# Optimization experiments

Measured on AMD Instinct MI355X. Metric: run time of the kernel, lower is better.

Reference implementation:

```python
import jax, jax.numpy as jnp
import numpy as np

H = 32; D = 128; HID = 4096       # heads, head_dim, hidden
DOFF = 1024; BD = 32; T = DOFF + BD  # prefill tokens, decode batch, total tokens
MAXKV = 513; R = 16; NA = 4       # kv-cache slots, lora rank, num adapters
SCALE = 1.0 / float(np.sqrt(D))


def _add_lora(y, x, wa, wb, segment):
    # segmented (multi-tenant) LoRA: y[t] += x[t] @ A[aid(t)] @ B[aid(t)]
    t = x.shape[0]
    aid = jnp.clip(jnp.searchsorted(segment, jnp.arange(t), side='right') - 1, 0, NA - 1)
    oh = jax.nn.one_hot(aid, NA, dtype=x.dtype)           # [t, NA]
    u = jnp.einsum('th,ahr->atr', x, wa)                  # [NA, t, R]
    v = jnp.einsum('atr,arh->ath', u, wb)                 # [NA, t, HID]
    return y + jnp.einsum('ta,ath->th', oh, v)


def setup_inputs() -> dict:
    key = jax.random.key(0)
    ks = jax.random.split(key, 16)
    f = lambda k, s: (jax.random.normal(k, s, dtype=jnp.float32) * 0.02)
    inp = {
        'hidden_states': f(ks[0], (T, HID)),
        'Wq': f(ks[1], (HID, HID)), 'Wk': f(ks[2], (HID, HID)),
        'Wv': f(ks[3], (HID, HID)), 'Wo': f(ks[4], (HID, HID)),
        'wa_q': f(ks[5], (NA, HID, R)), 'wb_q': f(ks[6], (NA, R, HID)),
        'wa_k': f(ks[7], (NA, HID, R)), 'wb_k': f(ks[8], (NA, R, HID)),
        'wa_v': f(ks[9], (NA, HID, R)), 'wb_v': f(ks[10], (NA, R, HID)),
        'wa_o': f(ks[11], (NA, HID, R)), 'wb_o': f(ks[12], (NA, R, HID)),
        'k_cache': f(ks[13], (BD, MAXKV, H, D)),
        'v_cache': f(ks[14], (BD, MAXKV, H, D)),
        'indptr': jnp.array([0, 200, 456, 800, 1024], dtype=jnp.int32),
        'segment': jnp.array([0, 300, 600, 900, 1056], dtype=jnp.int32),
        'kv_lens': jax.random.randint(ks[15], (BD,), 0, 512, dtype=jnp.int32),
    }
    return inp


def reference(hidden_states, Wq, Wk, Wv, Wo, wa_q, wb_q, wa_k, wb_k, wa_v, wb_v,
              wa_o, wb_o, k_cache, v_cache, indptr, segment, kv_lens):
    # qkv proj + segmented LoRA add
    qp = _add_lora(hidden_states @ Wq, hidden_states, wa_q, wb_q, segment)
    kp = _add_lora(hidden_states @ Wk, hidden_states, wa_k, wb_k, segment)
    vp = _add_lora(hidden_states @ Wv, hidden_states, wa_v, wb_v, segment)

    # ---- ragged prefill attention (causal within each sequence) ----
    q = qp[:DOFF].reshape(DOFF, H, D)
    k = kp[:DOFF].reshape(DOFF, H, D)
    v = vp[:DOFF].reshape(DOFF, H, D)
    idx = jnp.arange(DOFF)
    seg = jnp.searchsorted(indptr, idx, side='right') - 1   # sequence id per token
    m = (seg[:, None] == seg[None, :]) & (idx[None, :] <= idx[:, None])
    s = jnp.einsum('qhd,khd->hqk', q, k) * SCALE
    p = jax.nn.softmax(jnp.where(m[None], s, -1e9), axis=-1)
    out_p = jnp.einsum('hqk,khd->qhd', p, v).reshape(DOFF, HID)

    # ---- paged decode attention (append new kv, attend over cache) ----
    qd = qp[DOFF:].reshape(BD, H, D)
    kd = kp[DOFF:].reshape(BD, H, D)
    vd = vp[DOFF:].reshape(BD, H, D)
    b = jnp.arange(BD)
    kc = k_cache.at[b, kv_lens].set(kd)
    vc = v_cache.at[b, kv_lens].set(vd)
    lens = kv_lens + 1
    md = jnp.arange(MAXKV)[None, :] < lens[:, None]          # [BD, MAXKV]
    sd = jnp.einsum('bhd,bkhd->bhk', qd, kc) * SCALE
    pd = jax.nn.softmax(jnp.where(md[:, None, :], sd, -1e9), axis=-1)
    out_d = jnp.einsum('bhk,bkhd->bhd', pd, vc).reshape(BD, HID)

    attn = jnp.concatenate([out_p, out_d], axis=0)           # [T, HID]
    o = _add_lora(attn @ Wo, attn, wa_o, wb_o, segment)
    return o
```

## Files before the change

kernel.cpp:

```cpp
#include <hip/hip_runtime.h>
#include <hip/hip_bf16.h>

#define H_     32
#define D_     128
#define HID_   4096
#define DOFF_  1024
#define BD_    32
#define T_     1056
#define MAXKV_ 513
#define R_     16
#define NA_    4
#define SCALE_ 0.08838834764831845f

typedef __attribute__((ext_vector_type(8))) short short8;
typedef __attribute__((ext_vector_type(4))) float f32x4;

__device__ __forceinline__ float toF(float x) { return x; }
__device__ __forceinline__ float toF(__hip_bfloat16 x) { return __bfloat162float(x); }
__device__ __forceinline__ void storev(float* p, float v) { *p = v; }
__device__ __forceinline__ void storev(__hip_bfloat16* p, float v) { *p = __float2bfloat16(v); }

__device__ __forceinline__ void gload16(const void* g, void* l) {
  __builtin_amdgcn_global_load_lds(
      (const __attribute__((address_space(1))) unsigned int*)g,
      (__attribute__((address_space(3))) unsigned int*)l, 16, 0, 0);
}

__device__ __forceinline__ void load4(const float* p, float* v) {
  float4 t = *(const float4*)p;
  v[0] = t.x; v[1] = t.y; v[2] = t.z; v[3] = t.w;
}
__device__ __forceinline__ void load4(const __hip_bfloat16* p, float* v) {
  short4 t = *(const short4*)p;
  const __hip_bfloat16* e = (const __hip_bfloat16*)&t;
  v[0] = toF(e[0]); v[1] = toF(e[1]); v[2] = toF(e[2]); v[3] = toF(e[3]);
}

__global__ __launch_bounds__(256) void cast_bf16_kernel(
    const float* __restrict__ X, __hip_bfloat16* __restrict__ Y, int n4) {
  int i = blockIdx.x * 256 + threadIdx.x;
  if (i >= n4) return;
  float4 v = ((const float4*)X)[i];
  __hip_bfloat16 o[4] = {__float2bfloat16(v.x), __float2bfloat16(v.y),
                         __float2bfloat16(v.z), __float2bfloat16(v.w)};
  *(short4*)(Y + (size_t)i * 4) = *(short4*)o;
}

__global__ __launch_bounds__(256) void transpose_cast4_kernel(
    const float* __restrict__ W0, const float* __restrict__ W1,
    const float* __restrict__ W2, const float* __restrict__ W3,
    __hip_bfloat16* __restrict__ WT4) {
  __shared__ float tile[64][65];
  const float* W = blockIdx.z == 0 ? W0 : (blockIdx.z == 1 ? W1
                   : (blockIdx.z == 2 ? W2 : W3));
  __hip_bfloat16* WT = WT4 + (size_t)blockIdx.z * HID_ * HID_;
  int tx = threadIdx.x & 15;
  int ty = threadIdx.x >> 4;
  int r0 = blockIdx.y * 64, c0 = blockIdx.x * 64;
#pragma unroll
  for (int s = 0; s < 64; s += 16) {
    float4 v = *(const float4*)(W + (size_t)(r0 + ty + s) * HID_ + c0 + tx * 4);
    tile[ty + s][tx * 4 + 0] = v.x;
    tile[ty + s][tx * 4 + 1] = v.y;
    tile[ty + s][tx * 4 + 2] = v.z;
    tile[ty + s][tx * 4 + 3] = v.w;
  }
  __syncthreads();
#pragma unroll
  for (int s = 0; s < 64; s += 16) {
    int c = ty + s;
    __hip_bfloat16 o[4];
#pragma unroll
    for (int e = 0; e < 4; ++e) o[e] = __float2bfloat16(tile[tx * 4 + e][c]);
    *(short4*)(WT + (size_t)(c0 + c) * HID_ + r0 + tx * 4) = *(short4*)o;
  }
}

template <typename XT>
__global__ __launch_bounds__(256) void lora_u_kernel(
    const XT* __restrict__ X, const float* __restrict__ WA0,
    const float* __restrict__ WA1, const float* __restrict__ WA2,
    const int* __restrict__ segment, float* __restrict__ U0,
    float* __restrict__ U1, float* __restrict__ U2) {
  int t = blockIdx.x;
  int tid = threadIdx.x;
  const float* WA = blockIdx.y == 0 ? WA0 : (blockIdx.y == 1 ? WA1 : WA2);
  float* U = blockIdx.y == 0 ? U0 : (blockIdx.y == 1 ? U1 : U2);

  int aid = 0;
#pragma unroll
  for (int i = 1; i < NA_; ++i)
    if (t >= segment[i]) aid = i;

  const XT* x = X + (size_t)t * HID_;
  const float* wa = WA + (size_t)aid * HID_ * R_;

  float part[R_];
#pragma unroll
  for (int r = 0; r < R_; ++r) part[r] = 0.f;

  for (int h = tid * 4; h < HID_; h += 1024) {
    float xv[4];
    load4(x + h, xv);
#pragma unroll
    for (int e = 0; e < 4; ++e) {
      const float* w = wa + (size_t)(h + e) * R_;
#pragma unroll
      for (int r = 0; r < R_; ++r) part[r] += xv[e] * w[r];
    }
  }

  __shared__ float red[256][R_ + 1];
#pragma unroll
  for (int r = 0; r < R_; ++r) red[tid][r] = part[r];
  __syncthreads();
  for (int s = 128; s > 0; s >>= 1) {
    if (tid < s) {
#pragma unroll
      for (int r = 0; r < R_; ++r) red[tid][r] += red[tid + s][r];
    }
    __syncthreads();
  }
  if (tid < R_) U[(size_t)t * R_ + tid] = red[0][tid];
}

template <typename OUT_T>
__global__ __launch_bounds__(256) void gemm_bf16_lora_kernel(
    const __hip_bfloat16* __restrict__ Xb, const __hip_bfloat16* __restrict__ WT4,
    const float* __restrict__ U0, const float* __restrict__ U1,
    const float* __restrict__ U2, const float* __restrict__ B0,
    const float* __restrict__ B1, const float* __restrict__ B2,
    const int* __restrict__ segment, OUT_T* __restrict__ Y0,
    OUT_T* __restrict__ Y1, OUT_T* __restrict__ Y2, int Trows) {
  __shared__ __hip_bfloat16 As[128 * 32];
  __shared__ __hip_bfloat16 Bs[128 * 32];

  const int nwg = gridDim.x * gridDim.y;
  const int flat = blockIdx.y * gridDim.x + blockIdx.x;
  const int swz = (flat & 7) * (nwg >> 3) + (flat >> 3);
  const int bx = swz % gridDim.x;
  const int by = swz / gridDim.x;
  const int w = bx >> 5;
  const int n0 = (bx & 31) * 128;
  const int m0 = by * 128;

  const __hip_bfloat16* WT = WT4 + (size_t)w * HID_ * HID_;
  const float* U = w == 0 ? U0 : (w == 1 ? U1 : U2);
  const float* BMAT = w == 0 ? B0 : (w == 1 ? B1 : B2);
  OUT_T* Y = w == 0 ? Y0 : (w == 1 ? Y1 : Y2);

  const int tid = threadIdx.x;
  const int lane = tid & 63;
  const int wave = tid >> 6;
  const int wr = (wave >> 1) * 64;
  const int wc = (wave & 1) * 64;

  const int srow = tid >> 2;
  const int sel = (tid & 3) * 8;
  int ar0 = m0 + srow;      if (ar0 >= Trows) ar0 = Trows - 1;
  int ar1 = m0 + srow + 64; if (ar1 >= Trows) ar1 = Trows - 1;
  const __hip_bfloat16* gA0 = Xb + (size_t)ar0 * HID_ + sel;
  const __hip_bfloat16* gA1 = Xb + (size_t)ar1 * HID_ + sel;
  const __hip_bfloat16* gB0 = WT + (size_t)(n0 + srow) * HID_ + sel;
  const __hip_bfloat16* gB1 = WT + (size_t)(n0 + srow + 64) * HID_ + sel;
  __hip_bfloat16* lA = As + tid * 8;
  __hip_bfloat16* lB = Bs + tid * 8;

  const int lrow = lane & 15;
  const int lk = (lane >> 4) * 8;
  const __hip_bfloat16* fA = As + (wr + lrow) * 32 + lk;
  const __hip_bfloat16* fB = Bs + (wc + lrow) * 32 + lk;

  f32x4 acc[4][4] = {};

  for (int k0 = 0; k0 < HID_; k0 += 32) {
    gload16(gA0, lA);
    gload16(gA1, lA + 2048);
    gload16(gB0, lB);
    gload16(gB1, lB + 2048);
    gA0 += 32; gA1 += 32; gB0 += 32; gB1 += 32;
    __syncthreads();
    short8 a[4], b[4];
#pragma unroll
    for (int mi = 0; mi < 4; ++mi) a[mi] = *(const short8*)(fA + mi * 512);
#pragma unroll
    for (int ni = 0; ni < 4; ++ni) b[ni] = *(const short8*)(fB + ni * 512);
#pragma unroll
    for (int mi = 0; mi < 4; ++mi)
#pragma unroll
      for (int ni = 0; ni < 4; ++ni)
        acc[mi][ni] = __builtin_amdgcn_mfma_f32_16x16x32_bf16(a[mi], b[ni], acc[mi][ni], 0, 0, 0);
    __syncthreads();
  }

  const int crow = (lane >> 4) * 4;
  const int ccol = lane & 15;
#pragma unroll
  for (int mi = 0; mi < 4; ++mi) {
    const int tb = m0 + wr + mi * 16 + crow;
#pragma unroll
    for (int i = 0; i < 4; ++i) {
      const int t = tb + i;
      if (t >= Trows) continue;
      int aid = 0;
#pragma unroll
      for (int s = 1; s < NA_; ++s)
        if (t >= segment[s]) aid = s;
      const float* ub = U + (size_t)t * R_;
      const float* bb = BMAT + (size_t)aid * R_ * HID_;
#pragma unroll
      for (int ni = 0; ni < 4; ++ni) {
        const int n = n0 + wc + ni * 16 + ccol;
        float v = acc[mi][ni][i];
        const float* bc = bb + n;
#pragma unroll
        for (int r = 0; r < R_; ++r) v += ub[r] * bc[(size_t)r * HID_];
        storev(Y + (size_t)t * HID_ + n, v);
      }
    }
  }
}

#define QB 64
#define KB 32

__global__ __launch_bounds__(256) void attn_prefill_mfma_kernel(
    const __hip_bfloat16* __restrict__ qp, const __hip_bfloat16* __restrict__ kp,
    const __hip_bfloat16* __restrict__ vp, const int* __restrict__ indptr,
    __hip_bfloat16* __restrict__ attn) {
  __shared__ __hip_bfloat16 Klds[KB * 128];
  __shared__ __hip_bfloat16 Vt[128 * 40];
  __shared__ __hip_bfloat16 Plds[4][16 * 40];

  const int nwg = gridDim.x * gridDim.y;
  const int flat = blockIdx.y * gridDim.x + blockIdx.x;
  const int swz = (flat & 7) * (nwg >> 3) + (flat >> 3);
  const int q0 = (swz % gridDim.x) * QB;
  const int h = swz / gridDim.x;

  const int tid = threadIdx.x;
  const int lane = tid & 63;
  const int wave = tid >> 6;
  const int g = lane >> 4;
  const int lc = lane & 15;

  int qrows[4], qstart[4];
#pragma unroll
  for (int i = 0; i < 4; ++i) {
    int q = q0 + wave * 16 + g * 4 + i;
    qrows[i] = q;
    int s0 = 0;
#pragma unroll
    for (int j = 1; j < NA_; ++j)
      if (q >= indptr[j]) s0 = indptr[j];
    qstart[i] = s0;
  }

  short8 aq[4];
  {
    const __hip_bfloat16* qrow = qp + (size_t)(q0 + wave * 16 + lc) * HID_ + h * D_;
#pragma unroll
    for (int dc = 0; dc < 4; ++dc)
      aq[dc] = *(const short8*)(qrow + dc * 32 + g * 8);
  }

  float mrow[4], lrow[4];
#pragma unroll
  for (int i = 0; i < 4; ++i) { mrow[i] = -1e30f; lrow[i] = 0.f; }
  f32x4 o[8] = {};

  int ks0 = 0;
#pragma unroll
  for (int j = 1; j < NA_; ++j)
    if (q0 >= indptr[j]) ks0 = indptr[j];
  const int kt0 = ks0 & ~(KB - 1);

  const int sr = tid >> 4;
  const int sc = tid & 15;

  for (int kt = kt0; kt < q0 + QB; kt += KB) {
    gload16(kp + (size_t)(kt + sr) * HID_ + h * D_ + ((sc ^ (sr & 7)) * 8),
            Klds + tid * 8);
    gload16(kp + (size_t)(kt + 16 + sr) * HID_ + h * D_ + ((sc ^ (sr & 7)) * 8),
            Klds + 2048 + tid * 8);
    {
      short8 v0 = *(const short8*)(vp + (size_t)(kt + sr) * HID_ + h * D_ + sc * 8);
      short8 v1 = *(const short8*)(vp + (size_t)(kt + 16 + sr) * HID_ + h * D_ + sc * 8);
      const __hip_bfloat16* e0 = (const __hip_bfloat16*)&v0;
      const __hip_bfloat16* e1 = (const __hip_bfloat16*)&v1;
#pragma unroll
      for (int e = 0; e < 8; ++e) {
        Vt[(sc * 8 + e) * 40 + sr] = e0[e];
        Vt[(sc * 8 + e) * 40 + sr + 16] = e1[e];
      }
    }
    __syncthreads();

    f32x4 s0v = {}, s1v = {};
#pragma unroll
    for (int dc = 0; dc < 4; ++dc) {
      const int cb = dc * 4 + g;
      short8 bk0 = *(const short8*)(Klds + lc * 128 + ((cb ^ (lc & 7)) * 8));
      short8 bk1 = *(const short8*)(Klds + (16 + lc) * 128 + ((cb ^ (lc & 7)) * 8));
      s0v = __builtin_amdgcn_mfma_f32_16x16x32_bf16(aq[dc], bk0, s0v, 0, 0, 0);
      s1v = __builtin_amdgcn_mfma_f32_16x16x32_bf16(aq[dc], bk1, s1v, 0, 0, 0);
    }

    const int kl0 = kt + lc, kl1 = kt + 16 + lc;
#pragma unroll
    for (int i = 0; i < 4; ++i) {
      float sm0 = s0v[i] * SCALE_;
      float sm1 = s1v[i] * SCALE_;
      bool v0ok = (kl0 >= qstart[i]) && (kl0 <= qrows[i]);
      bool v1ok = (kl1 >= qstart[i]) && (kl1 <= qrows[i]);
      float mx = fmaxf(v0ok ? sm0 : -1e30f, v1ok ? sm1 : -1e30f);
#pragma unroll
      for (int off = 1; off < 16; off <<= 1)
        mx = fmaxf(mx, __shfl_xor(mx, off));
      float mnew = fmaxf(mrow[i], mx);
      float alpha = __expf(mrow[i] - mnew);
      float p0 = v0ok ? __expf(sm0 - mnew) : 0.f;
      float p1 = v1ok ? __expf(sm1 - mnew) : 0.f;
      lrow[i] = lrow[i] * alpha + p0 + p1;
      mrow[i] = mnew;
#pragma unroll
      for (int dc = 0; dc < 8; ++dc) o[dc][i] *= alpha;
      Plds[wave][(g * 4 + i) * 40 + lc] = __float2bfloat16(p0);
      Plds[wave][(g * 4 + i) * 40 + 16 + lc] = __float2bfloat16(p1);
    }

    asm volatile("s_waitcnt lgkmcnt(0)" ::: "memory");

    short8 ap = *(const short8*)(&Plds[wave][lc * 40 + g * 8]);
#pragma unroll
    for (int dc = 0; dc < 8; ++dc) {
      short8 bv = *(const short8*)(&Vt[(dc * 16 + lc) * 40 + g * 8]);
      o[dc] = __builtin_amdgcn_mfma_f32_16x16x32_bf16(ap, bv, o[dc], 0, 0, 0);
    }
    __syncthreads();
  }

#pragma unroll
  for (int i = 0; i < 4; ++i) {
    float l = lrow[i];
#pragma unroll
    for (int off = 1; off < 16; off <<= 1) l += __shfl_xor(l, off);
    lrow[i] = 1.f / l;
  }
#pragma unroll
  for (int dc = 0; dc < 8; ++dc)
#pragma unroll
    for (int i = 0; i < 4; ++i)
      attn[(size_t)qrows[i] * HID_ + h * D_ + dc * 16 + lc] =
          __float2bfloat16(o[dc][i] * lrow[i]);
}

__global__ __launch_bounds__(256) void attn_decode_kernel(
    const __hip_bfloat16* __restrict__ qp, const __hip_bfloat16* __restrict__ kp,
    const __hip_bfloat16* __restrict__ vp, const float* __restrict__ kcache,
    const float* __restrict__ vcache, const int* __restrict__ kv_lens,
    __hip_bfloat16* __restrict__ attn) {
  int h = blockIdx.x;
  int b = blockIdx.y;
  int wave = threadIdx.x >> 6;
  int lane = threadIdx.x & 63;
  int t = DOFF_ + b;

  const __hip_bfloat16* qptr = qp + (size_t)t * HID_ + h * D_;
  float q0 = toF(qptr[lane]), q1 = toF(qptr[lane + 64]);
  int len = kv_lens[b];

  int cnt = len + 1;
  int chunk = (cnt + 3) >> 2;
  int ks = wave * chunk;
  int ke = ks + chunk; if (ke > cnt) ke = cnt;

  float m = -1e30f, l = 0.f, acc0 = 0.f, acc1 = 0.f;
  for (int k = ks; k < ke; ++k) {
    float kv0, kv1, vv0, vv1;
    if (k == len) {
      const __hip_bfloat16* kptr = kp + (size_t)t * HID_ + h * D_;
      const __hip_bfloat16* vptr = vp + (size_t)t * HID_ + h * D_;
      kv0 = toF(kptr[lane]); kv1 = toF(kptr[lane + 64]);
      vv0 = toF(vptr[lane]); vv1 = toF(vptr[lane + 64]);
    } else {
      size_t base = (((size_t)b * MAXKV_ + k) * H_ + h) * D_;
      kv0 = kcache[base + lane]; kv1 = kcache[base + lane + 64];
      vv0 = vcache[base + lane]; vv1 = vcache[base + lane + 64];
    }
    float s = q0 * kv0 + q1 * kv1;
#pragma unroll
    for (int off = 32; off > 0; off >>= 1) s += __shfl_xor(s, off);
    s *= SCALE_;
    float mnew = fmaxf(m, s);
    float alpha = __expf(m - mnew);
    float p = __expf(s - mnew);
    acc0 = acc0 * alpha + p * vv0;
    acc1 = acc1 * alpha + p * vv1;
    l = l * alpha + p;
    m = mnew;
  }

  __shared__ float sm[4], sl[4], sacc[4][128];
  if (lane == 0) { sm[wave] = m; sl[wave] = l; }
  sacc[wave][lane] = acc0;
  sacc[wave][lane + 64] = acc1;
  __syncthreads();
  if (wave == 0) {
    float M = fmaxf(fmaxf(sm[0], sm[1]), fmaxf(sm[2], sm[3]));
    float L = 0.f, A0 = 0.f, A1 = 0.f;
#pragma unroll
    for (int w = 0; w < 4; ++w) {
      float sc = __expf(sm[w] - M);
      L += sl[w] * sc;
      A0 += sacc[w][lane] * sc;
      A1 += sacc[w][lane + 64] * sc;
    }
    float inv = 1.f / L;
    __hip_bfloat16* outp = attn + (size_t)t * HID_ + h * D_;
    storev(outp + lane, A0 * inv);
    storev(outp + lane + 64, A1 * inv);
  }
}

extern "C" void kernel_launch(void* const* d_in, const int* in_sizes, int n_in,
                              void* d_out, int out_size, void* d_ws, size_t ws_size,
                              hipStream_t stream) {
  const float* hidden  = (const float*)d_in[0];
  const float* Wq      = (const float*)d_in[1];
  const float* Wk      = (const float*)d_in[2];
  const float* Wv      = (const float*)d_in[3];
  const float* Wo      = (const float*)d_in[4];
  const float* wa_q    = (const float*)d_in[5];
  const float* wb_q    = (const float*)d_in[6];
  const float* wa_k    = (const float*)d_in[7];
  const float* wb_k    = (const float*)d_in[8];
  const float* wa_v    = (const float*)d_in[9];
  const float* wb_v    = (const float*)d_in[10];
  const float* wa_o    = (const float*)d_in[11];
  const float* wb_o    = (const float*)d_in[12];
  const float* k_cache = (const float*)d_in[13];
  const float* v_cache = (const float*)d_in[14];
  const int*   indptr  = (const int*)d_in[15];
  const int*   segment = (const int*)d_in[16];
  const int*   kv_lens = (const int*)d_in[17];
  float* out = (float*)d_out;

  const size_t PROJ = (size_t)T_ * HID_;
  __hip_bfloat16* Xb    = (__hip_bfloat16*)d_ws;
  __hip_bfloat16* qp    = Xb + PROJ;
  __hip_bfloat16* kp    = qp + PROJ;
  __hip_bfloat16* vp    = kp + PROJ;
  __hip_bfloat16* attnb = vp + PROJ;
  __hip_bfloat16* WT4   = attnb + PROJ;
  float* u_q = (float*)(WT4 + 4 * (size_t)HID_ * HID_);
  float* u_k = u_q + (size_t)T_ * R_;
  float* u_v = u_k + (size_t)T_ * R_;
  float* u_o = u_v + (size_t)T_ * R_;

  const int n4 = (int)(PROJ / 4);

  cast_bf16_kernel<<<(n4 + 255) / 256, 256, 0, stream>>>(hidden, Xb, n4);
  transpose_cast4_kernel<<<dim3(HID_ / 64, HID_ / 64, 4), 256, 0, stream>>>(
      Wq, Wk, Wv, Wo, WT4);
  lora_u_kernel<float><<<dim3(T_, 3), 256, 0, stream>>>(
      hidden, wa_q, wa_k, wa_v, segment, u_q, u_k, u_v);

  gemm_bf16_lora_kernel<__hip_bfloat16><<<dim3(96, 9), 256, 0, stream>>>(
      Xb, WT4, u_q, u_k, u_v, wb_q, wb_k, wb_v, segment, qp, kp, vp, T_);

  attn_prefill_mfma_kernel<<<dim3(DOFF_ / QB, H_), 256, 0, stream>>>(qp, kp, vp, indptr, attnb);
  attn_decode_kernel<<<dim3(H_, BD_), 256, 0, stream>>>(qp, kp, vp, k_cache, v_cache,
                                                        kv_lens, attnb);

  lora_u_kernel<__hip_bfloat16><<<dim3(T_, 1), 256, 0, stream>>>(
      attnb, wa_o, wa_o, wa_o, segment, u_o, u_o, u_o);
  gemm_bf16_lora_kernel<float><<<dim3(32, 9), 256, 0, stream>>>(
      attnb, WT4 + 3 * (size_t)HID_ * HID_, u_o, u_o, u_o, wb_o, wb_o, wb_o,
      segment, out, out, out, T_);
}
```

Measured before the change: 751.7 us.

## Double-buffer LDS tiles in bf16 LoRA GEMM to overlap loads with MFMA

Splits the shared-memory A/B tiles into two buffers and restructures the K loop so the global-to-LDS load of the next 32-wide K slice is issued before the MFMA compute on the current slice. This cuts one of the two barriers per K step and lets memory latency hide behind matrix math. It doubles LDS use per block, which may lower occupancy. The correctness of async global_load_lds relative to the barrier waits depends on the compiler inserting vmcnt waits at __syncthreads.

Result: slower. 788.3 us (+4.9%).

```diff
diff --git a/kernel.cpp b/kernel.cpp
--- a/kernel.cpp
+++ b/kernel.cpp
@@ -132,8 +132,8 @@
     const float* __restrict__ B1, const float* __restrict__ B2,
     const int* __restrict__ segment, OUT_T* __restrict__ Y0,
     OUT_T* __restrict__ Y1, OUT_T* __restrict__ Y2, int Trows) {
-  __shared__ __hip_bfloat16 As[128 * 32];
-  __shared__ __hip_bfloat16 Bs[128 * 32];
+  __shared__ __hip_bfloat16 As[2][128 * 32];
+  __shared__ __hip_bfloat16 Bs[2][128 * 32];
 
   const int nwg = gridDim.x * gridDim.y;
   const int flat = blockIdx.y * gridDim.x + blockIdx.x;
@@ -163,35 +163,53 @@
   const __hip_bfloat16* gA1 = Xb + (size_t)ar1 * HID_ + sel;
   const __hip_bfloat16* gB0 = WT + (size_t)(n0 + srow) * HID_ + sel;
   const __hip_bfloat16* gB1 = WT + (size_t)(n0 + srow + 64) * HID_ + sel;
-  __hip_bfloat16* lA = As + tid * 8;
-  __hip_bfloat16* lB = Bs + tid * 8;
 
   const int lrow = lane & 15;
   const int lk = (lane >> 4) * 8;
-  const __hip_bfloat16* fA = As + (wr + lrow) * 32 + lk;
-  const __hip_bfloat16* fB = Bs + (wc + lrow) * 32 + lk;
+  const int fAo = (wr + lrow) * 32 + lk;
+  const int fBo = (wc + lrow) * 32 + lk;
 
   f32x4 acc[4][4] = {};
 
-  for (int k0 = 0; k0 < HID_; k0 += 32) {
-    gload16(gA0, lA);
-    gload16(gA1, lA + 2048);
-    gload16(gB0, lB);
-    gload16(gB1, lB + 2048);
-    gA0 += 32; gA1 += 32; gB0 += 32; gB1 += 32;
+#define STAGE_(B, koff)                                   \
+  do {                                                    \
+    gload16(gA0 + (koff), As[B] + tid * 8);               \
+    gload16(gA1 + (koff), As[B] + 2048 + tid * 8);        \
+    gload16(gB0 + (koff), Bs[B] + tid * 8);               \
+    gload16(gB1 + (koff), Bs[B] + 2048 + tid * 8);        \
+  } while (0)
+
+#define COMPUTE_(B)                                                          \
+  do {                                                                       \
+    short8 a[4], b[4];                                                       \
+    _Pragma("unroll") for (int mi = 0; mi < 4; ++mi)                         \
+        a[mi] = *(const short8*)(As[B] + fAo + mi * 512);                    \
+    _Pragma("unroll") for (int ni = 0; ni < 4; ++ni)                         \
+        b[ni] = *(const short8*)(Bs[B] + fBo + ni * 512);                    \
+    _Pragma("unroll") for (int mi = 0; mi < 4; ++mi)                         \
+        _Pragma("unroll") for (int ni = 0; ni < 4; ++ni)                     \
+            acc[mi][ni] = __builtin_amdgcn_mfma_f32_16x16x32_bf16(           \
+                a[mi], b[ni], acc[mi][ni], 0, 0, 0);                         \
+  } while (0)
+
+  STAGE_(0, 0);
+  __syncthreads();
+
+  for (int k0 = 0; k0 < HID_ - 64; k0 += 64) {
+    STAGE_(1, k0 + 32);
+    COMPUTE_(0);
     __syncthreads();
-    short8 a[4], b[4];
-#pragma unroll
-    for (int mi = 0; mi < 4; ++mi) a[mi] = *(const short8*)(fA + mi * 512);
-#pragma unroll
-    for (int ni = 0; ni < 4; ++ni) b[ni] = *(const short8*)(fB + ni * 512);
-#pragma unroll
-    for (int mi = 0; mi < 4; ++mi)
-#pragma unroll
-      for (int ni = 0; ni < 4; ++ni)
-        acc[mi][ni] = __builtin_amdgcn_mfma_f32_16x16x32_bf16(a[mi], b[ni], acc[mi][ni], 0, 0, 0);
+    STAGE_(0, k0 + 64);
+    COMPUTE_(1);
     __syncthreads();
   }
+  STAGE_(1, HID_ - 32);
+  COMPUTE_(0);
+  __syncthreads();
+  COMPUTE_(1);
+
+#undef STAGE_
+#undef COMPUTE_
 
   const int crow = (lane >> 4) * 4;
   const int ccol = lane & 15;
```

## Double GEMM K-tile to 64 with XOR-swizzled LDS and XCD-aware block mapping

Applied to the files above, without the earlier changes.

The bf16 QKV GEMM now stages 64-wide K slices per iteration instead of 32, halving the number of barrier pairs per tile. The LDS layout is XOR-swizzled by row so MFMA fragment reads avoid bank conflicts. Workgroup-to-tile remapping is changed so each XCD owns a contiguous band of N columns and walks over M. The cost is doubled LDS per block, which may lower occupancy.

After: 936.2 us. 1.25x slower.

```diff
diff --git a/kernel.cpp b/kernel.cpp
--- a/kernel.cpp
+++ b/kernel.cpp
@@ -132,14 +132,17 @@
     const float* __restrict__ B1, const float* __restrict__ B2,
     const int* __restrict__ segment, OUT_T* __restrict__ Y0,
     OUT_T* __restrict__ Y1, OUT_T* __restrict__ Y2, int Trows) {
-  __shared__ __hip_bfloat16 As[128 * 32];
-  __shared__ __hip_bfloat16 Bs[128 * 32];
-
-  const int nwg = gridDim.x * gridDim.y;
-  const int flat = blockIdx.y * gridDim.x + blockIdx.x;
-  const int swz = (flat & 7) * (nwg >> 3) + (flat >> 3);
-  const int bx = swz % gridDim.x;
-  const int by = swz / gridDim.x;
+  __shared__ __hip_bfloat16 As[128 * 64];
+  __shared__ __hip_bfloat16 Bs[128 * 64];
+
+  const int nx = gridDim.x;
+  const int ny = gridDim.y;
+  const int flat = blockIdx.y * nx + blockIdx.x;
+  const int xcd = flat & 7;
+  const int pos = flat >> 3;
+  const int bands = nx >> 3;
+  const int bx = xcd * bands + pos / ny;
+  const int by = pos % ny;
   const int w = bx >> 5;
   const int n0 = (bx & 31) * 128;
   const int m0 = by * 128;
@@ -155,41 +158,49 @@
   const int wr = (wave >> 1) * 64;
   const int wc = (wave & 1) * 64;
 
-  const int srow = tid >> 2;
-  const int sel = (tid & 3) * 8;
-  int ar0 = m0 + srow;      if (ar0 >= Trows) ar0 = Trows - 1;
-  int ar1 = m0 + srow + 64; if (ar1 >= Trows) ar1 = Trows - 1;
-  const __hip_bfloat16* gA0 = Xb + (size_t)ar0 * HID_ + sel;
-  const __hip_bfloat16* gA1 = Xb + (size_t)ar1 * HID_ + sel;
-  const __hip_bfloat16* gB0 = WT + (size_t)(n0 + srow) * HID_ + sel;
-  const __hip_bfloat16* gB1 = WT + (size_t)(n0 + srow + 64) * HID_ + sel;
-  __hip_bfloat16* lA = As + tid * 8;
-  __hip_bfloat16* lB = Bs + tid * 8;
+  const int srow = tid >> 3;
+  const int schunk = tid & 7;
+  const int sw = (schunk ^ (srow & 7)) * 8;
+
+  const __hip_bfloat16* gAsrc[4];
+  const __hip_bfloat16* gBsrc[4];
+#pragma unroll
+  for (int i = 0; i < 4; ++i) {
+    int ra = m0 + i * 32 + srow; if (ra >= Trows) ra = Trows - 1;
+    gAsrc[i] = Xb + (size_t)ra * HID_ + sw;
+    gBsrc[i] = WT + (size_t)(n0 + i * 32 + srow) * HID_ + sw;
+  }
 
   const int lrow = lane & 15;
-  const int lk = (lane >> 4) * 8;
-  const __hip_bfloat16* fA = As + (wr + lrow) * 32 + lk;
-  const __hip_bfloat16* fB = Bs + (wc + lrow) * 32 + lk;
+  const int g = lane >> 4;
+  const int sx = lrow & 7;
 
   f32x4 acc[4][4] = {};
 
-  for (int k0 = 0; k0 < HID_; k0 += 32) {
-    gload16(gA0, lA);
-    gload16(gA1, lA + 2048);
-    gload16(gB0, lB);
-    gload16(gB1, lB + 2048);
-    gA0 += 32; gA1 += 32; gB0 += 32; gB1 += 32;
+  for (int k0 = 0; k0 < HID_; k0 += 64) {
+#pragma unroll
+    for (int i = 0; i < 4; ++i) gload16(gAsrc[i] + k0, As + i * 2048 + tid * 8);
+#pragma unroll
+    for (int i = 0; i < 4; ++i) gload16(gBsrc[i] + k0, Bs + i * 2048 + tid * 8);
     __syncthreads();
-    short8 a[4], b[4];
-#pragma unroll
-    for (int mi = 0; mi < 4; ++mi) a[mi] = *(const short8*)(fA + mi * 512);
-#pragma unroll
-    for (int ni = 0; ni < 4; ++ni) b[ni] = *(const short8*)(fB + ni * 512);
-#pragma unroll
-    for (int mi = 0; mi < 4; ++mi)
+#pragma unroll
+    for (int ks = 0; ks < 2; ++ks) {
+      short8 a[4], b[4];
+#pragma unroll
+      for (int mi = 0; mi < 4; ++mi)
+        a[mi] = *(const short8*)(As + (wr + lrow + mi * 16) * 64 +
+                                 ((ks * 4 + g) ^ sx) * 8);
 #pragma unroll
       for (int ni = 0; ni < 4; ++ni)
-        acc[mi][ni] = __builtin_amdgcn_mfma_f32_16x16x32_bf16(a[mi], b[ni], acc[mi][ni], 0, 0, 0);
+        b[ni] = *(const short8*)(Bs + (wc + lrow + ni * 16) * 64 +
+                                 ((ks * 4 + g) ^ sx) * 8);
+#pragma unroll
+      for (int mi = 0; mi < 4; ++mi)
+#pragma unroll
+        for (int ni = 0; ni < 4; ++ni)
+          acc[mi][ni] = __builtin_amdgcn_mfma_f32_16x16x32_bf16(
+              a[mi], b[ni], acc[mi][ni], 0, 0, 0);
+    }
     __syncthreads();
   }
 
```

## Split-K the projection GEMMs and move the LoRA epilogue to a reduce kernel

Applied to the files above, without the earlier changes.

The bf16 GEMMs now split the K dimension across gridDim.z (2 for QKV, 4 for the output projection) and write fp32 partial tiles to workspace. A new reduce kernel sums the partials and applies the segmented LoRA B-term with vectorized loads before writing the final output. The aim is more workgroups to fill the CUs, since the output GEMM had only 288 tiles, and removing the strided scalar LoRA epilogue from the GEMM. In exchange it adds large fp32 partial-buffer traffic (about 52MB for QKV) and extra kernel launches.

After: 727.1 us. 3.3% less time.

```diff
diff --git a/kernel.cpp b/kernel.cpp
--- a/kernel.cpp
+++ b/kernel.cpp
@@ -124,14 +124,9 @@
   if (tid < R_) U[(size_t)t * R_ + tid] = red[0][tid];
 }
 
-template <typename OUT_T>
-__global__ __launch_bounds__(256) void gemm_bf16_lora_kernel(
+__global__ __launch_bounds__(256) void gemm_bf16_part_kernel(
     const __hip_bfloat16* __restrict__ Xb, const __hip_bfloat16* __restrict__ WT4,
-    const float* __restrict__ U0, const float* __restrict__ U1,
-    const float* __restrict__ U2, const float* __restrict__ B0,
-    const float* __restrict__ B1, const float* __restrict__ B2,
-    const int* __restrict__ segment, OUT_T* __restrict__ Y0,
-    OUT_T* __restrict__ Y1, OUT_T* __restrict__ Y2, int Trows) {
+    float* __restrict__ part, int Trows) {
   __shared__ __hip_bfloat16 As[128 * 32];
   __shared__ __hip_bfloat16 Bs[128 * 32];
 
@@ -144,10 +139,11 @@
   const int n0 = (bx & 31) * 128;
   const int m0 = by * 128;
 
+  const int klen = HID_ / gridDim.z;
+  const int kbase = blockIdx.z * klen;
+
   const __hip_bfloat16* WT = WT4 + (size_t)w * HID_ * HID_;
-  const float* U = w == 0 ? U0 : (w == 1 ? U1 : U2);
-  const float* BMAT = w == 0 ? B0 : (w == 1 ? B1 : B2);
-  OUT_T* Y = w == 0 ? Y0 : (w == 1 ? Y1 : Y2);
+  float* P = part + ((size_t)w * gridDim.z + blockIdx.z) * ((size_t)T_ * HID_);
 
   const int tid = threadIdx.x;
   const int lane = tid & 63;
@@ -159,10 +155,10 @@
   const int sel = (tid & 3) * 8;
   int ar0 = m0 + srow;      if (ar0 >= Trows) ar0 = Trows - 1;
   int ar1 = m0 + srow + 64; if (ar1 >= Trows) ar1 = Trows - 1;
-  const __hip_bfloat16* gA0 = Xb + (size_t)ar0 * HID_ + sel;
-  const __hip_bfloat16* gA1 = Xb + (size_t)ar1 * HID_ + sel;
-  const __hip_bfloat16* gB0 = WT + (size_t)(n0 + srow) * HID_ + sel;
-  const __hip_bfloat16* gB1 = WT + (size_t)(n0 + srow + 64) * HID_ + sel;
+  const __hip_bfloat16* gA0 = Xb + (size_t)ar0 * HID_ + kbase + sel;
+  const __hip_bfloat16* gA1 = Xb + (size_t)ar1 * HID_ + kbase + sel;
+  const __hip_bfloat16* gB0 = WT + (size_t)(n0 + srow) * HID_ + kbase + sel;
+  const __hip_bfloat16* gB1 = WT + (size_t)(n0 + srow + 64) * HID_ + kbase + sel;
   __hip_bfloat16* lA = As + tid * 8;
   __hip_bfloat16* lB = Bs + tid * 8;
 
@@ -173,7 +169,7 @@
 
   f32x4 acc[4][4] = {};
 
-  for (int k0 = 0; k0 < HID_; k0 += 32) {
+  for (int k0 = 0; k0 < klen; k0 += 32) {
     gload16(gA0, lA);
     gload16(gA1, lA + 2048);
     gload16(gB0, lB);
@@ -202,22 +198,62 @@
     for (int i = 0; i < 4; ++i) {
       const int t = tb + i;
       if (t >= Trows) continue;
-      int aid = 0;
-#pragma unroll
-      for (int s = 1; s < NA_; ++s)
-        if (t >= segment[s]) aid = s;
-      const float* ub = U + (size_t)t * R_;
-      const float* bb = BMAT + (size_t)aid * R_ * HID_;
 #pragma unroll
       for (int ni = 0; ni < 4; ++ni) {
         const int n = n0 + wc + ni * 16 + ccol;
-        float v = acc[mi][ni][i];
-        const float* bc = bb + n;
-#pragma unroll
-        for (int r = 0; r < R_; ++r) v += ub[r] * bc[(size_t)r * HID_];
-        storev(Y + (size_t)t * HID_ + n, v);
+        P[(size_t)t * HID_ + n] = acc[mi][ni][i];
       }
     }
+  }
+}
+
+template <typename OUT_T, int NS>
+__global__ __launch_bounds__(256) void reduce_lora_kernel(
+    const float* __restrict__ part, const float* __restrict__ U0,
+    const float* __restrict__ U1, const float* __restrict__ U2,
+    const float* __restrict__ B0, const float* __restrict__ B1,
+    const float* __restrict__ B2, const int* __restrict__ segment,
+    OUT_T* __restrict__ Y0, OUT_T* __restrict__ Y1, OUT_T* __restrict__ Y2) {
+  const int t = blockIdx.x;
+  const int mat = blockIdx.y;
+  const int tid = threadIdx.x;
+
+  const float* U = mat == 0 ? U0 : (mat == 1 ? U1 : U2);
+  const float* B = mat == 0 ? B0 : (mat == 1 ? B1 : B2);
+  OUT_T* Y = mat == 0 ? Y0 : (mat == 1 ? Y1 : Y2);
+
+  int aid = 0;
+#pragma unroll
+  for (int i = 1; i < NA_; ++i)
+    if (t >= segment[i]) aid = i;
+
+  float u[R_];
+#pragma unroll
+  for (int r = 0; r < R_; ++r) u[r] = U[(size_t)t * R_ + r];
+
+  const size_t pstride = (size_t)T_ * HID_;
+  const float* pbase = part + (size_t)mat * NS * pstride + (size_t)t * HID_;
+  const float* bbase = B + (size_t)aid * R_ * HID_;
+  OUT_T* ybase = Y + (size_t)t * HID_;
+
+  for (int j = tid; j < HID_ / 4; j += 256) {
+    const int n = j * 4;
+    float4 acc = *(const float4*)(pbase + n);
+#pragma unroll
+    for (int s = 1; s < NS; ++s) {
+      float4 p = *(const float4*)(pbase + s * pstride + n);
+      acc.x += p.x; acc.y += p.y; acc.z += p.z; acc.w += p.w;
+    }
+#pragma unroll
+    for (int r = 0; r < R_; ++r) {
+      float4 b = *(const float4*)(bbase + (size_t)r * HID_ + n);
+      acc.x += u[r] * b.x; acc.y += u[r] * b.y;
+      acc.z += u[r] * b.z; acc.w += u[r] * b.w;
+    }
+    storev(ybase + n + 0, acc.x);
+    storev(ybase + n + 1, acc.y);
+    storev(ybase + n + 2, acc.z);
+    storev(ybase + n + 3, acc.w);
   }
 }
 
@@ -457,6 +493,7 @@
   float* u_k = u_q + (size_t)T_ * R_;
   float* u_v = u_k + (size_t)T_ * R_;
   float* u_o = u_v + (size_t)T_ * R_;
+  float* partb = u_o + (size_t)T_ * R_;
 
   const int n4 = (int)(PROJ / 4);
 
@@ -466,8 +503,9 @@
   lora_u_kernel<float><<<dim3(T_, 3), 256, 0, stream>>>(
       hidden, wa_q, wa_k, wa_v, segment, u_q, u_k, u_v);
 
-  gemm_bf16_lora_kernel<__hip_bfloat16><<<dim3(96, 9), 256, 0, stream>>>(
-      Xb, WT4, u_q, u_k, u_v, wb_q, wb_k, wb_v, segment, qp, kp, vp, T_);
+  gemm_bf16_part_kernel<<<dim3(96, 9, 2), 256, 0, stream>>>(Xb, WT4, partb, T_);
+  reduce_lora_kernel<__hip_bfloat16, 2><<<dim3(T_, 3), 256, 0, stream>>>(
+      partb, u_q, u_k, u_v, wb_q, wb_k, wb_v, segment, qp, kp, vp);
 
   attn_prefill_mfma_kernel<<<dim3(DOFF_ / QB, H_), 256, 0, stream>>>(qp, kp, vp, indptr, attnb);
   attn_decode_kernel<<<dim3(H_, BD_), 256, 0, stream>>>(qp, kp, vp, k_cache, v_cache,
@@ -475,7 +513,8 @@
 
   lora_u_kernel<__hip_bfloat16><<<dim3(T_, 1), 256, 0, stream>>>(
       attnb, wa_o, wa_o, wa_o, segment, u_o, u_o, u_o);
-  gemm_bf16_lora_kernel<float><<<dim3(32, 9), 256, 0, stream>>>(
-      attnb, WT4 + 3 * (size_t)HID_ * HID_, u_o, u_o, u_o, wb_o, wb_o, wb_o,
-      segment, out, out, out, T_);
-}
+  gemm_bf16_part_kernel<<<dim3(32, 9, 4), 256, 0, stream>>>(
+      attnb, WT4 + 3 * (size_t)HID_ * HID_, partb, T_);
+  reduce_lora_kernel<float, 4><<<dim3(T_, 1), 256, 0, stream>>>(
+      partb, u_o, u_o, u_o, wb_o, wb_o, wb_o, segment, out, out, out);
+}
```
